# Kernel tuning notes

Measured on AMD Instinct MI355X. Metric: run time of the kernel, lower is better.

Reference implementation:

```python
import jax, jax.numpy as jnp
import numpy as np

CPV = 64  # cpv_size; output_size = CPV*(CPV+1)//2 = 2080

def _tri_indices(cpv):
    # Reproduce the torch nested-loop scatter order:
    # for idx_x in range(cpv): for idx_y in range(cpv-idx_x): col = cpv-1-idx_y
    rows = np.repeat(np.arange(cpv), cpv - np.arange(cpv))
    cols = np.concatenate([np.arange(cpv - 1, i - 1, -1) for i in range(cpv)])
    return jnp.asarray(rows), jnp.asarray(cols)


def setup_inputs() -> dict:
    key = jax.random.key(0)
    ks = jax.random.split(key, 12)
    B, D_in, H, L = 8192, 1024, 2048, CPV * (CPV + 1) // 2
    s = lambda fan_in: 1.0 / np.sqrt(fan_in)
    return {
        "x":   jax.random.normal(ks[0], (B, D_in), jnp.float32),
        "W1":  jax.random.uniform(ks[1], (D_in, H), jnp.float32, -s(D_in), s(D_in)),
        "b1":  jnp.zeros((H,), jnp.float32),
        "W2":  jax.random.uniform(ks[2], (H, H), jnp.float32, -s(H), s(H)),
        "b2":  jnp.zeros((H,), jnp.float32),
        "W21": jax.random.uniform(ks[3], (H, H), jnp.float32, -s(H), s(H)),
        "b21": jnp.zeros((H,), jnp.float32),
        "W22": jax.random.uniform(ks[4], (H, H), jnp.float32, -s(H), s(H)),
        "b22": jnp.zeros((H,), jnp.float32),
        "W3":  jax.random.uniform(ks[5], (H, L), jnp.float32, -s(H), s(H)),
        "b3":  jnp.zeros((L,), jnp.float32),
    }


def reference(x, W1, b1, W2, b2, W21, b21, W22, b22, W3, b3):
    lrelu = lambda t: jax.nn.leaky_relu(t, 0.01)
    h = lrelu(x @ W1 + b1)
    h = lrelu(h @ W2 + b2)
    h = lrelu(h @ W21 + b21)
    h = lrelu(h @ W22 + b22)
    y = h @ W3 + b3  # [B, L] with L = CPV*(CPV+1)//2
    rows, cols = _tri_indices(CPV)
    is_diag = rows == cols  # diagonal entries are abs'ed (negated when <= 0)
    vals = jnp.where(is_diag[None, :] & (y <= 0), -y, y)
    B = y.shape[0]
    M = jnp.zeros((B, CPV, CPV), y.dtype).at[:, rows, cols].set(vals)
    return jnp.transpose(M, (1, 2, 0))  # torch stacks per-example matrices on dim=2
```

## Files before the change

kernel.cpp:

```cpp
#include <hip/hip_runtime.h>
#include <hip/hip_bf16.h>
#include <stdint.h>

typedef short short8 __attribute__((ext_vector_type(8)));
typedef float f32x4  __attribute__((ext_vector_type(4)));

typedef __attribute__((address_space(1))) uint32_t u32_g;
typedef __attribute__((address_space(3))) uint32_t u32_l;

#define BM 128
#define BN 128
#define BK 64

__device__ __forceinline__ void gld_lds16(const void* g, const void* l) {
  __builtin_amdgcn_global_load_lds((u32_g*)(uintptr_t)g, (u32_l*)(uintptr_t)l, 16, 0, 0);
}

template <int FINAL>
__global__ __launch_bounds__(256) void gemm_k(
    const __hip_bfloat16* __restrict__ A,
    const __hip_bfloat16* __restrict__ BT,
    const float* __restrict__ bias,
    __hip_bfloat16* __restrict__ Cb,
    float* __restrict__ Cf,
    const int* __restrict__ tbl,
    int K, int Nreal)
{
  __shared__ __attribute__((aligned(16))) char smem[33792];

  const int tid  = threadIdx.x;
  const int lane = tid & 63;
  const int l15  = lane & 15;
  const int quad = lane >> 4;
  const int wave = tid >> 6;
  const int wm   = (wave >> 1) << 6;
  const int wn   = (wave & 1) << 6;

  const int bm = blockIdx.x * BM;
  const int bn = blockIdx.y * BN;

  const __hip_bfloat16* ag[4];
  const __hip_bfloat16* bg[4];
  uint32_t lofs[4];
#pragma unroll
  for (int c = 0; c < 4; ++c) {
    int ci   = tid + 256 * c;
    int row  = ci >> 3;
    int chk  = ci & 7;
    int gchk = chk ^ (row & 7);
    ag[c]   = A  + (size_t)(bm + row) * K + gchk * 8;
    bg[c]   = BT + (size_t)(bn + row) * K + gchk * 8;
    lofs[c] = (uint32_t)ci * 16u;
  }

  f32x4 acc[4][4];
#pragma unroll
  for (int i = 0; i < 4; ++i)
#pragma unroll
    for (int j = 0; j < 4; ++j)
      acc[i][j] = (f32x4){0.f, 0.f, 0.f, 0.f};

  const int nk = K >> 6;
  for (int kt = 0; kt < nk; ++kt) {
#pragma unroll
    for (int c = 0; c < 4; ++c) {
      gld_lds16(ag[c], smem + lofs[c]);
      gld_lds16(bg[c], smem + 16384 + lofs[c]);
      ag[c] += BK;
      bg[c] += BK;
    }
    __syncthreads();
#pragma unroll
    for (int ks = 0; ks < 2; ++ks) {
      short8 af[4], bf[4];
      const int cf = ks * 4 + quad;
#pragma unroll
      for (int i = 0; i < 4; ++i) {
        int m  = wm + i * 16 + l15;
        int sc = cf ^ (m & 7);
        af[i]  = *(const short8*)(smem + m * 128 + sc * 16);
      }
#pragma unroll
      for (int j = 0; j < 4; ++j) {
        int n  = wn + j * 16 + l15;
        int sc = cf ^ (n & 7);
        bf[j]  = *(const short8*)(smem + 16384 + n * 128 + sc * 16);
      }
#pragma unroll
      for (int i = 0; i < 4; ++i)
#pragma unroll
        for (int j = 0; j < 4; ++j)
          acc[i][j] = __builtin_amdgcn_mfma_f32_16x16x32_bf16(af[i], bf[j], acc[i][j], 0, 0, 0);
    }
    __syncthreads();
  }

  if (FINAL == 0) {
#pragma unroll
    for (int j = 0; j < 4; ++j) {
      int   n  = wn + j * 16 + l15;
      float bv = bias[bn + n];
#pragma unroll
      for (int i = 0; i < 4; ++i) {
        int m0 = wm + i * 16 + quad * 4;
#pragma unroll
        for (int r = 0; r < 4; ++r) {
          float v = acc[i][j][r] + bv;
          v = (v > 0.f) ? v : 0.01f * v;
          *(__hip_bfloat16*)(smem + (m0 + r) * 264 + n * 2) = __float2bfloat16(v);
        }
      }
    }
    __syncthreads();
    const int rr = tid >> 4;
    const int cb = (tid & 15) * 16;
#pragma unroll
    for (int p = 0; p < 8; ++p) {
      int row = p * 16 + rr;
      short8 v = *(const short8*)(smem + row * 264 + cb);
      *reinterpret_cast<short8*>((char*)Cb + ((size_t)(bm + row) * 2048 + bn) * 2 + cb) = v;
    }
  } else {
#pragma unroll
    for (int j = 0; j < 4; ++j) {
      int n = bn + wn + j * 16 + l15;
      if (n < Nreal) {
        float bv   = bias[n];
        int  code  = tbl[n];
        int  dst   = code & 4095;
        bool diag  = (code & 4096) != 0;
        int  mir   = ((dst & 63) << 6) | (dst >> 6);
        const f32x4 z = (f32x4){0.f, 0.f, 0.f, 0.f};
#pragma unroll
        for (int i = 0; i < 4; ++i) {
          int m0 = bm + wm + i * 16 + quad * 4;
          f32x4 pk;
#pragma unroll
          for (int r = 0; r < 4; ++r) {
            float v = acc[i][j][r] + bv;
            if (diag) v = fabsf(v);
            pk[r] = v;
          }
          *reinterpret_cast<f32x4*>(Cf + (size_t)dst * 8192 + m0) = pk;
          if (!diag)
            *reinterpret_cast<f32x4*>(Cf + (size_t)mir * 8192 + m0) = z;
        }
      }
    }
  }
}

__global__ void transpose_k(const float* __restrict__ in,
                            __hip_bfloat16* __restrict__ out,
                            int K, int N)
{
  __shared__ __hip_bfloat16 t[32][33];
  const int n0 = blockIdx.x * 32;
  const int k0 = blockIdx.y * 32;
  const int tx = threadIdx.x, ty = threadIdx.y;
  const __hip_bfloat16 zero = __float2bfloat16(0.f);
#pragma unroll
  for (int r = 0; r < 32; r += 8) {
    int k = k0 + ty + r, n = n0 + tx;
    t[ty + r][tx] = (n < N) ? __float2bfloat16(in[(size_t)k * N + n]) : zero;
  }
  __syncthreads();
#pragma unroll
  for (int r = 0; r < 32; r += 8) {
    int n = n0 + ty + r;
    out[(size_t)n * K + k0 + tx] = t[tx][ty + r];
  }
}

__global__ void cvt_k(const float* __restrict__ in,
                      __hip_bfloat16* __restrict__ out, int n)
{
  int i = (blockIdx.x * 256 + threadIdx.x) * 4;
  if (i >= n) return;
  float4 v = *reinterpret_cast<const float4*>(in + i);
  union { unsigned short us[4]; uint2 v2; } pk;
  __hip_bfloat16 h;
  h = __float2bfloat16(v.x); pk.us[0] = *reinterpret_cast<unsigned short*>(&h);
  h = __float2bfloat16(v.y); pk.us[1] = *reinterpret_cast<unsigned short*>(&h);
  h = __float2bfloat16(v.z); pk.us[2] = *reinterpret_cast<unsigned short*>(&h);
  h = __float2bfloat16(v.w); pk.us[3] = *reinterpret_cast<unsigned short*>(&h);
  *reinterpret_cast<uint2*>(out + i) = pk.v2;
}

__global__ void table_k(int* __restrict__ tbl)
{
  int l = blockIdx.x * 64 + threadIdx.x;
  if (l >= 2080) return;
  int r = 0, s = 0;
  while (s + (64 - r) <= l) { s += 64 - r; ++r; }
  int c = 63 - (l - s);
  tbl[l] = (r * 64 + c) | ((r == c) ? 4096 : 0);
}

extern "C" void kernel_launch(void* const* d_in, const int* in_sizes, int n_in,
                              void* d_out, int out_size, void* d_ws, size_t ws_size,
                              hipStream_t stream)
{
  const float* x   = (const float*)d_in[0];
  const float* W1  = (const float*)d_in[1];
  const float* b1  = (const float*)d_in[2];
  const float* W2  = (const float*)d_in[3];
  const float* b2  = (const float*)d_in[4];
  const float* W21 = (const float*)d_in[5];
  const float* b21 = (const float*)d_in[6];
  const float* W22 = (const float*)d_in[7];
  const float* b22 = (const float*)d_in[8];
  const float* W3  = (const float*)d_in[9];
  const float* b3  = (const float*)d_in[10];
  float* out = (float*)d_out;

  char* ws = (char*)d_ws;
  __hip_bfloat16* act0 = (__hip_bfloat16*)(ws);
  __hip_bfloat16* act1 = (__hip_bfloat16*)(ws + ((size_t)32 << 20));
  __hip_bfloat16* xb   = act1;
  __hip_bfloat16* W1T  = (__hip_bfloat16*)(ws + ((size_t)64 << 20));
  __hip_bfloat16* W2T  = (__hip_bfloat16*)(ws + ((size_t)68 << 20));
  __hip_bfloat16* W21T = (__hip_bfloat16*)(ws + ((size_t)76 << 20));
  __hip_bfloat16* W22T = (__hip_bfloat16*)(ws + ((size_t)84 << 20));
  __hip_bfloat16* W3T  = (__hip_bfloat16*)(ws + ((size_t)92 << 20));
  int*            tbl  = (int*)(ws + ((size_t)101 << 20));

  table_k<<<33, 64, 0, stream>>>(tbl);

  cvt_k<<<8192, 256, 0, stream>>>(x, xb, 8192 * 1024);

  dim3 tb(32, 8);
  transpose_k<<<dim3(64, 32), tb, 0, stream>>>(W1,  W1T,  1024, 2048);
  transpose_k<<<dim3(64, 64), tb, 0, stream>>>(W2,  W2T,  2048, 2048);
  transpose_k<<<dim3(64, 64), tb, 0, stream>>>(W21, W21T, 2048, 2048);
  transpose_k<<<dim3(64, 64), tb, 0, stream>>>(W22, W22T, 2048, 2048);
  transpose_k<<<dim3(68, 64), tb, 0, stream>>>(W3,  W3T,  2048, 2080);

  gemm_k<0><<<dim3(64, 16), 256, 0, stream>>>(xb,   W1T,  b1,  act0, nullptr, nullptr, 1024, 2048);
  gemm_k<0><<<dim3(64, 16), 256, 0, stream>>>(act0, W2T,  b2,  act1, nullptr, nullptr, 2048, 2048);
  gemm_k<0><<<dim3(64, 16), 256, 0, stream>>>(act1, W21T, b21, act0, nullptr, nullptr, 2048, 2048);
  gemm_k<0><<<dim3(64, 16), 256, 0, stream>>>(act0, W22T, b22, act1, nullptr, nullptr, 2048, 2048);
  gemm_k<1><<<dim3(64, 17), 256, 0, stream>>>(act1, W3T,  b3,  nullptr, out,  tbl,     2048, 2080);
}
```

Baseline: 635.4 us.

## Double-buffer LDS tiles in GEMM and store epilogue directly to global

The GEMM main loop now uses two 32 KB LDS buffers. The next K-tile's global-to-LDS loads are issued before the MFMAs on the current tile, and one barrier per iteration is removed, so memory latency can overlap with compute. The bf16 epilogue drops the LDS-staged, 16-byte coalesced store and writes each 2-byte element straight to global memory. The cost is double the LDS footprint, which may lower occupancy, and narrower, less coalesced output stores.

```diff
diff --git a/kernel.cpp b/kernel.cpp
--- a/kernel.cpp
+++ b/kernel.cpp
@@ -26,7 +26,7 @@
     const int* __restrict__ tbl,
     int K, int Nreal)
 {
-  __shared__ __attribute__((aligned(16))) char smem[33792];
+  __shared__ __attribute__((aligned(16))) char smem[65536];
 
   const int tid  = threadIdx.x;
   const int lane = tid & 63;
@@ -61,15 +61,30 @@
       acc[i][j] = (f32x4){0.f, 0.f, 0.f, 0.f};
 
   const int nk = K >> 6;
+
+#pragma unroll
+  for (int c = 0; c < 4; ++c) {
+    gld_lds16(ag[c], smem + lofs[c]);
+    gld_lds16(bg[c], smem + 16384 + lofs[c]);
+    ag[c] += BK;
+    bg[c] += BK;
+  }
+  __syncthreads();
+
   for (int kt = 0; kt < nk; ++kt) {
-#pragma unroll
-    for (int c = 0; c < 4; ++c) {
-      gld_lds16(ag[c], smem + lofs[c]);
-      gld_lds16(bg[c], smem + 16384 + lofs[c]);
-      ag[c] += BK;
-      bg[c] += BK;
-    }
-    __syncthreads();
+    const char* rb = smem + (kt & 1) * 32768;
+    char*       sb = smem + ((kt + 1) & 1) * 32768;
+
+    if (kt + 1 < nk) {
+#pragma unroll
+      for (int c = 0; c < 4; ++c) {
+        gld_lds16(ag[c], sb + lofs[c]);
+        gld_lds16(bg[c], sb + 16384 + lofs[c]);
+        ag[c] += BK;
+        bg[c] += BK;
+      }
+    }
+
 #pragma unroll
     for (int ks = 0; ks < 2; ++ks) {
       short8 af[4], bf[4];
@@ -78,13 +93,13 @@
       for (int i = 0; i < 4; ++i) {
         int m  = wm + i * 16 + l15;
         int sc = cf ^ (m & 7);
-        af[i]  = *(const short8*)(smem + m * 128 + sc * 16);
+        af[i]  = *(const short8*)(rb + m * 128 + sc * 16);
       }
 #pragma unroll
       for (int j = 0; j < 4; ++j) {
         int n  = wn + j * 16 + l15;
         int sc = cf ^ (n & 7);
-        bf[j]  = *(const short8*)(smem + 16384 + n * 128 + sc * 16);
+        bf[j]  = *(const short8*)(rb + 16384 + n * 128 + sc * 16);
       }
 #pragma unroll
       for (int i = 0; i < 4; ++i)
@@ -96,29 +111,22 @@
   }
 
   if (FINAL == 0) {
-#pragma unroll
-    for (int j = 0; j < 4; ++j) {
-      int   n  = wn + j * 16 + l15;
-      float bv = bias[bn + n];
-#pragma unroll
-      for (int i = 0; i < 4; ++i) {
-        int m0 = wm + i * 16 + quad * 4;
-#pragma unroll
-        for (int r = 0; r < 4; ++r) {
-          float v = acc[i][j][r] + bv;
+    float bv[4];
+#pragma unroll
+    for (int j = 0; j < 4; ++j) bv[j] = bias[bn + wn + j * 16 + l15];
+#pragma unroll
+    for (int i = 0; i < 4; ++i) {
+#pragma unroll
+      for (int r = 0; r < 4; ++r) {
+        const size_t rowoff = (size_t)(bm + wm + i * 16 + quad * 4 + r) * 2048;
+#pragma unroll
+        for (int j = 0; j < 4; ++j) {
+          int n = bn + wn + j * 16 + l15;
+          float v = acc[i][j][r] + bv[j];
           v = (v > 0.f) ? v : 0.01f * v;
-          *(__hip_bfloat16*)(smem + (m0 + r) * 264 + n * 2) = __float2bfloat16(v);
+          Cb[rowoff + n] = __float2bfloat16(v);
         }
       }
-    }
-    __syncthreads();
-    const int rr = tid >> 4;
-    const int cb = (tid & 15) * 16;
-#pragma unroll
-    for (int p = 0; p < 8; ++p) {
-      int row = p * 16 + rr;
-      short8 v = *(const short8*)(smem + row * 264 + cb);
-      *reinterpret_cast<short8*>((char*)Cb + ((size_t)(bm + row) * 2048 + bn) * 2 + cb) = v;
     }
   } else {
 #pragma unroll
```

Measured after the change: 569.0 us (median of 2 runs). 10.5% less time.
